# Performance work log

Hardware: AMD Instinct MI355X
Metric: run time of the kernel (lower is better)

## Reference

```python
import jax, jax.numpy as jnp
import numpy as np
from jax import lax

NB_ITERS = 10
HS = 3        # nb_kerhalfsize
HS_LIF = 3    # nb_kerhalfsize_LIF
DN = ('NCDHW', 'OIDHW', 'NCDHW')


def std_kernel(sigma, halfsize):
    # sigma: (C,1,1,1) -> normalized Gaussian kernel (C,1,k,k,k)
    r = jnp.arange(-halfsize, halfsize + 1, dtype=jnp.float32)
    x, y, z = jnp.meshgrid(r, r, r, indexing='ij')  # (k,k,k)
    d2 = x ** 2 + y ** 2 + z ** 2
    sig2 = sigma.reshape(-1, 1, 1, 1) ** 2          # (C,1,1,1)
    ker = jnp.exp(-d2[None] / (2.0 * sig2))         # (C,k,k,k)
    ker = ker / (ker.sum(axis=(1, 2, 3), keepdims=True) + 1e-15)
    return ker[:, None]                              # (C,1,k,k,k)


def dconv(x, ker, halfsize):
    # depthwise (grouped, groups=C) 3D conv with 'same' zero padding
    C = x.shape[1]
    pad = [(halfsize, halfsize)] * 3
    return lax.conv_general_dilated(x, ker, window_strides=(1, 1, 1),
                                    padding=pad, feature_group_count=C,
                                    dimension_numbers=DN)


def setup_inputs() -> dict:
    key = jax.random.key(0)
    k1, k2 = jax.random.split(key)
    C = 4
    shape = (1, C, 96, 96, 96)
    o = jax.random.normal(k1, shape, dtype=jnp.float32)
    I = jax.random.uniform(k2, (1, 1, 96, 96, 96), dtype=jnp.float32)
    sigma2 = jnp.ones((C, 1, 1, 1), dtype=jnp.float32)
    sigma3 = jnp.ones((C, 1, 1, 1), dtype=jnp.float32)
    eta = jnp.ones((1,), dtype=jnp.float32)
    lam = jnp.ones((1,), dtype=jnp.float32) * 5.0
    mu = jnp.ones((1,), dtype=jnp.float32) * 5.0
    return {'o': o, 'I': I, 'sigma2': sigma2, 'sigma3': sigma3,
            'eta': eta, 'lam': lam, 'mu': mu}


def reference(o, I, sigma2, sigma3, eta, lam, mu):
    u = jax.nn.softmax(o / eta, axis=1)
    ker = std_kernel(sigma2, HS)
    ker_lif = std_kernel(sigma3, HS_LIF)
    # conv of the all-ones tensor is loop-invariant (boundary normalization)
    conv_ones = dconv(jnp.ones_like(u), ker_lif, HS_LIF)
    I2 = I ** 2
    for _ in range(NB_ITERS):
        uI = u * I
        C1 = dconv(uI, ker_lif, HS_LIF)
        C2 = dconv(u, ker_lif, HS_LIF)
        Cn = (C1 + 1e-6) / (C2 + 1e-6)
        Lif = (dconv(Cn ** 2, ker_lif, HS_LIF)
               - 2.0 * I * dconv(Cn, ker_lif, HS_LIF)
               + I2 * conv_ones)
        q = dconv(1.0 - 2.0 * u, ker, HS)
        u = jax.nn.softmax((o - mu * Lif - lam * q) / eta, axis=1)
    return u
```

## Files before the change

### kernel.cpp

```cpp
#include <hip/hip_runtime.h>
#include <math.h>

#define PLANE  9216
#define PLANE4 2304
#define VOL    884736
#define VOL4   221184
#define NC     4
#define K      7
#define HSR    3
#define SEGZ   8
#define NSEGZ  12
#define SEGZ4  16
#define NSEGZ4 6

#define YT     16
#define YTH    22
#define TPBYX  192
#define LINW   100
#define MIDW   108
#define NF4    528

__device__ __forceinline__ float4 f4zero() { return make_float4(0.f, 0.f, 0.f, 0.f); }
__device__ __forceinline__ float4 f4fma(float t, float4 a, float4 s) {
    s.x = fmaf(t, a.x, s.x); s.y = fmaf(t, a.y, s.y);
    s.z = fmaf(t, a.z, s.z); s.w = fmaf(t, a.w, s.w);
    return s;
}
__device__ __forceinline__ float4 f4fmasq(float t, float4 a, float4 s) {
    s.x = fmaf(t, a.x * a.x, s.x); s.y = fmaf(t, a.y * a.y, s.y);
    s.z = fmaf(t, a.z * a.z, s.z); s.w = fmaf(t, a.w * a.w, s.w);
    return s;
}
__device__ __forceinline__ float4 f4mul(float4 a, float4 b) {
    return make_float4(a.x * b.x, a.y * b.y, a.z * b.z, a.w * b.w);
}

__global__ void tables_kernel(const float* __restrict__ sigma2,
                              const float* __restrict__ sigma3,
                              float* __restrict__ taps2, float* __restrict__ taps3,
                              float* __restrict__ B2, float* __restrict__ B3)
{
    int t = threadIdx.x;
    if (t < 2 * NC) {
        int c = t % NC;
        const float* sig = (t < NC) ? sigma2 : sigma3;
        float* taps = (t < NC) ? taps2 : taps3;
        float sv = sig[c];
        float s2 = sv * sv;
        float w[K];
        float sum = 0.f;
        for (int j = 0; j < K; j++) {
            float d = (float)(j - HSR);
            w[j] = expf(-d * d / (2.f * s2));
            sum += w[j];
        }
        float inv = 1.f / sum;
        for (int j = 0; j < K; j++) taps[c * K + j] = w[j] * inv;
    }
    __syncthreads();
    for (int i = t; i < NC * 96; i += blockDim.x) {
        int c = i / 96, p = i % 96;
        float s2v = 0.f, s3v = 0.f;
        for (int j = 0; j < K; j++) {
            int q = p + j - HSR;
            if (q >= 0 && q < 96) { s2v += taps2[c * K + j]; s3v += taps3[c * K + j]; }
        }
        B2[i] = s2v;
        B3[i] = s3v;
    }
}

__global__ __launch_bounds__(256) void softmax_kernel(const float* __restrict__ a,
                                                      const float* __restrict__ eta,
                                                      float* __restrict__ u)
{
    int i = blockIdx.x * 256 + threadIdx.x;
    const float4* A = (const float4*)a;
    float4* U = (float4*)u;
    float inv_eta = 1.f / eta[0];
    float4 a0 = A[i], a1 = A[i + VOL4], a2 = A[i + 2 * VOL4], a3 = A[i + 3 * VOL4];
#define SM_COMP(f)                                                              \
    {                                                                           \
        float b0 = a0.f * inv_eta, b1 = a1.f * inv_eta;                         \
        float b2 = a2.f * inv_eta, b3 = a3.f * inv_eta;                         \
        float m = fmaxf(fmaxf(b0, b1), fmaxf(b2, b3));                          \
        float e0 = __expf(b0 - m), e1 = __expf(b1 - m);                         \
        float e2 = __expf(b2 - m), e3 = __expf(b3 - m);                         \
        float inv = 1.f / (e0 + e1 + e2 + e3);                                  \
        a0.f = e0 * inv; a1.f = e1 * inv; a2.f = e2 * inv; a3.f = e3 * inv;     \
    }
    SM_COMP(x) SM_COMP(y) SM_COMP(z) SM_COMP(w)
    U[i] = a0; U[i + VOL4] = a1; U[i + 2 * VOL4] = a2; U[i + 3 * VOL4] = a3;
}

__global__ __launch_bounds__(256) void pass1_z(const float* __restrict__ u,
                                               const float* __restrict__ I,
                                               const float* __restrict__ taps2,
                                               const float* __restrict__ taps3,
                                               float* __restrict__ a0, float* __restrict__ a1,
                                               float* __restrict__ a2)
{
    int p4 = blockIdx.x * 256 + threadIdx.x;
    int s  = blockIdx.y;
    int c  = blockIdx.z;
    int z0 = s * SEGZ;
    const float4* ub = (const float4*)(u + (size_t)c * VOL) + p4;
    const float4* Ib = (const float4*)I + p4;
    float t3[K], t2[K];
#pragma unroll
    for (int j = 0; j < K; j++) { t3[j] = taps3[c * K + j]; t2[j] = taps2[c * K + j]; }
    float4 wu[K], wui[K];
#pragma unroll
    for (int j = 0; j < K - 1; j++) {
        int z = z0 + j - HSR;
        float4 uv = f4zero(), iv = f4zero();
        if (z >= 0 && z < 96) { uv = ub[z * PLANE4]; iv = Ib[z * PLANE4]; }
        wu[j] = uv; wui[j] = f4mul(uv, iv);
    }
    float4* o0 = (float4*)(a0 + (size_t)c * VOL) + p4;
    float4* o1 = (float4*)(a1 + (size_t)c * VOL) + p4;
    float4* o2 = (float4*)(a2 + (size_t)c * VOL) + p4;
    for (int k = 0; k < SEGZ; k++) {
        int z = z0 + k, zl = z + HSR;
        float4 uv = f4zero(), iv = f4zero();
        if (zl < 96) { uv = ub[zl * PLANE4]; iv = Ib[zl * PLANE4]; }
        wu[K - 1] = uv; wui[K - 1] = f4mul(uv, iv);
        float4 s0 = f4zero(), s1 = f4zero(), s2 = f4zero();
#pragma unroll
        for (int j = 0; j < K; j++) {
            s0 = f4fma(t3[j], wui[j], s0);
            s1 = f4fma(t3[j], wu[j], s1);
            s2 = f4fma(t2[j], wu[j], s2);
        }
        o0[z * PLANE4] = s0;
        o1[z * PLANE4] = s1;
        o2[z * PLANE4] = s2;
#pragma unroll
        for (int j = 0; j < K - 1; j++) { wu[j] = wu[j + 1]; wui[j] = wui[j + 1]; }
    }
}

__global__ __launch_bounds__(TPBYX) void pass2_yx(const float* __restrict__ a0,
                                                  const float* __restrict__ a1,
                                                  const float* __restrict__ taps3,
                                                  float* __restrict__ Cn)
{
    __shared__ float lin[2][YTH * LINW];
    __shared__ float mid[2][YT * MIDW];
    int yt = blockIdx.x, z = blockIdx.y, c = blockIdx.z;
    int y0 = yt * YT, tid = threadIdx.x;
    size_t base = (size_t)c * VOL + (size_t)z * PLANE;
    {
        const float4* g0 = (const float4*)(a0 + base);
        const float4* g1 = (const float4*)(a1 + base);
#pragma unroll
        for (int i4 = tid; i4 < NF4; i4 += TPBYX) {
            int r = i4 / 24, k = i4 - r * 24;
            int gy = y0 - HSR + r;
            bool ok = (gy >= 0 && gy < 96);
            int gi = gy * 24 + k;
            float4 v0 = ok ? g0[gi] : f4zero();
            float4 v1 = ok ? g1[gi] : f4zero();
            int li = r * LINW + k * 4;
            *(float4*)&lin[0][li] = v0;
            *(float4*)&lin[1][li] = v1;
        }
    }
    if (tid < 128) {
        int r = tid >> 3, p = tid & 7;
        int idx = r * MIDW + (p < 4 ? p : 96 + p);
        mid[0][idx] = 0.f; mid[1][idx] = 0.f;
    }
    float t3[K];
#pragma unroll
    for (int j = 0; j < K; j++) t3[j] = taps3[c * K + j];
    __syncthreads();
    int r  = tid / 12;
    int xb = (tid - r * 12) * 8;
#pragma unroll
    for (int f = 0; f < 2; f++) {
        float4 mA = f4zero(), mB = f4zero();
#pragma unroll
        for (int j = 0; j < K; j++) {
            const float4* lp = (const float4*)&lin[f][(r + j) * LINW + xb];
            mA = f4fma(t3[j], lp[0], mA);
            mB = f4fma(t3[j], lp[1], mB);
        }
        float4* mp = (float4*)&mid[f][r * MIDW + 4 + xb];
        mp[0] = mA; mp[1] = mB;
    }
    __syncthreads();
    float outA[8], outB[8];
    {
        float wf[16];
#pragma unroll
        for (int f = 0; f < 2; f++) {
            const float4* wp = (const float4*)&mid[f][r * MIDW + xb];
            *(float4*)&wf[0]  = wp[0];
            *(float4*)&wf[4]  = wp[1];
            *(float4*)&wf[8]  = wp[2];
            *(float4*)&wf[12] = wp[3];
            float* dst = (f == 0) ? outA : outB;
#pragma unroll
            for (int k = 0; k < 8; k++) {
                float s = 0.f;
#pragma unroll
                for (int j = 0; j < K; j++) s = fmaf(t3[j], wf[k + j + 1], s);
                dst[k] = s;
            }
        }
    }
    int y = y0 + r;
    float co[8];
#pragma unroll
    for (int k = 0; k < 8; k++)
        co[k] = (outA[k] + 1e-6f) / (outB[k] + 1e-6f);
    float* cp = Cn + base + y * 96 + xb;
    *(float4*)cp       = *(float4*)&co[0];
    *(float4*)(cp + 4) = *(float4*)&co[4];
}

__global__ __launch_bounds__(128) void pass4_z(const float* __restrict__ Cn,
                                               const float* __restrict__ taps3,
                                               float* __restrict__ b0, float* __restrict__ b1)
{
    int p4 = blockIdx.x * 128 + threadIdx.x;
    int s  = blockIdx.y;
    int c  = blockIdx.z;
    int z0 = s * SEGZ4;
    const float4* ib = (const float4*)(Cn + (size_t)c * VOL) + p4;
    float t3[K];
#pragma unroll
    for (int j = 0; j < K; j++) t3[j] = taps3[c * K + j];
    float4 w[K];
#pragma unroll
    for (int j = 0; j < K - 1; j++) {
        int z = z0 + j - HSR;
        float4 v = f4zero();
        if (z >= 0 && z < 96) v = ib[z * PLANE4];
        w[j] = v;
    }
    float4* o0 = (float4*)(b0 + (size_t)c * VOL) + p4;
    float4* o1 = (float4*)(b1 + (size_t)c * VOL) + p4;
    for (int k = 0; k < SEGZ4; k++) {
        int z = z0 + k, zl = z + HSR;
        float4 v = f4zero();
        if (zl < 96) v = ib[zl * PLANE4];
        w[K - 1] = v;
        float4 s0 = f4zero(), s1 = f4zero();
#pragma unroll
        for (int j = 0; j < K; j++) {
            s0 = f4fma(t3[j], w[j], s0);
            s1 = f4fmasq(t3[j], w[j], s1);
        }
        o0[z * PLANE4] = s0;
        o1[z * PLANE4] = s1;
#pragma unroll
        for (int j = 0; j < K - 1; j++) w[j] = w[j + 1];
    }
}

__global__ __launch_bounds__(TPBYX) void pass5_yx(const float* __restrict__ cz0,
                                                  const float* __restrict__ cz1,
                                                  const float* __restrict__ a2,
                                                  const float* __restrict__ o,
                                                  const float* __restrict__ I,
                                                  const float* __restrict__ taps2,
                                                  const float* __restrict__ taps3,
                                                  const float* __restrict__ B2,
                                                  const float* __restrict__ B3,
                                                  const float* __restrict__ eta,
                                                  const float* __restrict__ lam,
                                                  const float* __restrict__ mu,
                                                  float* __restrict__ argb)
{
    __shared__ float lin[3][YTH * LINW];
    __shared__ float mid[3][YT * MIDW];
    int yt = blockIdx.x, z = blockIdx.y, c = blockIdx.z;
    int y0 = yt * YT, tid = threadIdx.x;
    size_t base = (size_t)c * VOL + (size_t)z * PLANE;
    {
        const float4* g0 = (const float4*)(cz0 + base);
        const float4* g1 = (const float4*)(cz1 + base);
        const float4* g2 = (const float4*)(a2 + base);
#pragma unroll
        for (int i4 = tid; i4 < NF4; i4 += TPBYX) {
            int r = i4 / 24, k = i4 - r * 24;
            int gy = y0 - HSR + r;
            bool ok = (gy >= 0 && gy < 96);
            int gi = gy * 24 + k;
            float4 v0 = ok ? g0[gi] : f4zero();
            float4 v1 = ok ? g1[gi] : f4zero();
            float4 v2 = ok ? g2[gi] : f4zero();
            int li = r * LINW + k * 4;
            *(float4*)&lin[0][li] = v0;
            *(float4*)&lin[1][li] = v1;
            *(float4*)&lin[2][li] = v2;
        }
    }
    if (tid < 128) {
        int r = tid >> 3, p = tid & 7;
        int idx = r * MIDW + (p < 4 ? p : 96 + p);
        mid[0][idx] = 0.f; mid[1][idx] = 0.f; mid[2][idx] = 0.f;
    }
    float t3[K], t2[K];
#pragma unroll
    for (int j = 0; j < K; j++) { t3[j] = taps3[c * K + j]; t2[j] = taps2[c * K + j]; }
    __syncthreads();
    int r  = tid / 12;
    int xb = (tid - r * 12) * 8;
#pragma unroll
    for (int f = 0; f < 3; f++) {
        const float* tp = (f < 2) ? t3 : t2;
        float4 mA = f4zero(), mB = f4zero();
#pragma unroll
        for (int j = 0; j < K; j++) {
            const float4* lp = (const float4*)&lin[f][(r + j) * LINW + xb];
            mA = f4fma(tp[j], lp[0], mA);
            mB = f4fma(tp[j], lp[1], mB);
        }
        float4* mp = (float4*)&mid[f][r * MIDW + 4 + xb];
        mp[0] = mA; mp[1] = mB;
    }
    __syncthreads();
    float d0[8], d1[8], s2[8];
    {
        float wf[16];
#pragma unroll
        for (int f = 0; f < 3; f++) {
            const float* tp = (f < 2) ? t3 : t2;
            const float4* wp = (const float4*)&mid[f][r * MIDW + xb];
            *(float4*)&wf[0]  = wp[0];
            *(float4*)&wf[4]  = wp[1];
            *(float4*)&wf[8]  = wp[2];
            *(float4*)&wf[12] = wp[3];
            float* dst = (f == 0) ? d0 : (f == 1) ? d1 : s2;
#pragma unroll
            for (int k = 0; k < 8; k++) {
                float s = 0.f;
#pragma unroll
                for (int j = 0; j < K; j++) s = fmaf(tp[j], wf[k + j + 1], s);
                dst[k] = s;
            }
        }
    }
    int y = y0 + r;
    int v = z * PLANE + y * 96 + xb;
    float inv_eta = 1.f / eta[0];
    float lamv = lam[0], muv = mu[0];
    float Bz3 = B3[c * 96 + z], By3 = B3[c * 96 + y];
    float Bz2 = B2[c * 96 + z], By2 = B2[c * 96 + y];
    float Bx3[8], Bx2[8], Ivv[8], ov[8];
    {
        const float4* bx3 = (const float4*)&B3[c * 96 + xb];
        *(float4*)&Bx3[0] = bx3[0]; *(float4*)&Bx3[4] = bx3[1];
        const float4* bx2 = (const float4*)&B2[c * 96 + xb];
        *(float4*)&Bx2[0] = bx2[0]; *(float4*)&Bx2[4] = bx2[1];
        const float4* ip = (const float4*)&I[v];
        *(float4*)&Ivv[0] = ip[0]; *(float4*)&Ivv[4] = ip[1];
        const float4* op = (const float4*)&o[(size_t)c * VOL + v];
        *(float4*)&ov[0] = op[0]; *(float4*)&ov[4] = op[1];
    }
    float res[8];
#pragma unroll
    for (int k = 0; k < 8; k++) {
        float Iv = Ivv[k];
        float cones = Bz3 * By3 * Bx3[k];
        float Lif = d1[k] - 2.f * Iv * d0[k] + Iv * Iv * cones;
        float qv  = fmaf(Bz2 * By2, Bx2[k], -2.f * s2[k]);
        res[k] = ov[k] - muv * Lif - lamv * qv;
    }
    float* ap = argb + base + y * 96 + xb;
    *(float4*)ap       = *(float4*)&res[0];
    *(float4*)(ap + 4) = *(float4*)&res[4];
}

extern "C" void kernel_launch(void* const* d_in, const int* in_sizes, int n_in,
                              void* d_out, int out_size, void* d_ws, size_t ws_size,
                              hipStream_t stream)
{
    const float* o      = (const float*)d_in[0];
    const float* I      = (const float*)d_in[1];
    const float* sigma2 = (const float*)d_in[2];
    const float* sigma3 = (const float*)d_in[3];
    const float* eta    = (const float*)d_in[4];
    const float* lam    = (const float*)d_in[5];
    const float* mu     = (const float*)d_in[6];
    float* u = (float*)d_out;

    float* wsf = (float*)d_ws;
    float* taps2 = wsf;
    float* taps3 = wsf + 32;
    float* B2    = wsf + 64;
    float* B3    = wsf + 64 + NC * 96;
    float* buf   = wsf + 1024;
    const size_t VCs = (size_t)NC * VOL;
    float* a0 = buf;
    float* a1 = buf + VCs;
    float* a2 = buf + 2 * VCs;
    float* Cn = buf + 3 * VCs;
    float* c0 = buf + 4 * VCs;
    float* c1 = buf + 5 * VCs;

    const dim3 grid1(PLANE4 / 256, NSEGZ, NC);
    const dim3 gridYX(96 / YT, 96, NC);
    const dim3 grid4(PLANE4 / 128, NSEGZ4, NC);
    const int gridV4 = VOL4 / 256;

    tables_kernel<<<1, 512, 0, stream>>>(sigma2, sigma3, taps2, taps3, B2, B3);
    softmax_kernel<<<gridV4, 256, 0, stream>>>(o, eta, u);
    for (int it = 0; it < 10; it++) {
        pass1_z<<<grid1, 256, 0, stream>>>(u, I, taps2, taps3, a0, a1, a2);
        pass2_yx<<<gridYX, TPBYX, 0, stream>>>(a0, a1, taps3, Cn);
        pass4_z<<<grid4, 128, 0, stream>>>(Cn, taps3, c0, c1);
        pass5_yx<<<gridYX, TPBYX, 0, stream>>>(c0, c1, a2, o, I, taps2, taps3,
                                               B2, B3, eta, lam, mu, a0);
        softmax_kernel<<<gridV4, 256, 0, stream>>>(a0, eta, u);
    }
}
```

Baseline: 714.9 us.

## Fuse y and x conv passes in registers, drop mid shared buffer

The separable y and x convolutions in the yx kernels now run in registers. Each thread accumulates a 16-wide y-convolved window straight from the padded line buffer, then applies the x taps, so the intermediate shared array and one barrier are gone. The line buffer gains zero halos on both sides to support this. The z-pass also moves to 256-thread blocks with 8-slice segments, which doubles the halo reloads per output. The per-thread y pass does 16 columns instead of 8, so it adds redundant FMAs and register pressure.

```diff
diff --git a/kernel.cpp b/kernel.cpp
--- a/kernel.cpp
+++ b/kernel.cpp
@@ -10,14 +10,11 @@
 #define HSR    3
 #define SEGZ   8
 #define NSEGZ  12
-#define SEGZ4  16
-#define NSEGZ4 6
 
 #define YT     16
 #define YTH    22
 #define TPBYX  192
-#define LINW   100
-#define MIDW   108
+#define LINW   108
 #define NF4    528
 
 __device__ __forceinline__ float4 f4zero() { return make_float4(0.f, 0.f, 0.f, 0.f); }
@@ -33,6 +30,36 @@
 }
 __device__ __forceinline__ float4 f4mul(float4 a, float4 b) {
     return make_float4(a.x * b.x, a.y * b.y, a.z * b.z, a.w * b.w);
+}
+
+__device__ __forceinline__ void conv_win(const float* __restrict__ linf,
+                                         const float* __restrict__ tp,
+                                         int r, int xb, float out[8])
+{
+    float acc[16];
+#pragma unroll
+    for (int i = 0; i < 16; i++) acc[i] = 0.f;
+#pragma unroll
+    for (int j = 0; j < K; j++) {
+        const float4* lp = (const float4*)&linf[(r + j) * LINW + xb];
+        float4 w0 = lp[0], w1 = lp[1], w2 = lp[2], w3 = lp[3];
+        float t = tp[j];
+        acc[0]  = fmaf(t, w0.x, acc[0]);  acc[1]  = fmaf(t, w0.y, acc[1]);
+        acc[2]  = fmaf(t, w0.z, acc[2]);  acc[3]  = fmaf(t, w0.w, acc[3]);
+        acc[4]  = fmaf(t, w1.x, acc[4]);  acc[5]  = fmaf(t, w1.y, acc[5]);
+        acc[6]  = fmaf(t, w1.z, acc[6]);  acc[7]  = fmaf(t, w1.w, acc[7]);
+        acc[8]  = fmaf(t, w2.x, acc[8]);  acc[9]  = fmaf(t, w2.y, acc[9]);
+        acc[10] = fmaf(t, w2.z, acc[10]); acc[11] = fmaf(t, w2.w, acc[11]);
+        acc[12] = fmaf(t, w3.x, acc[12]); acc[13] = fmaf(t, w3.y, acc[13]);
+        acc[14] = fmaf(t, w3.z, acc[14]); acc[15] = fmaf(t, w3.w, acc[15]);
+    }
+#pragma unroll
+    for (int k = 0; k < 8; k++) {
+        float s = 0.f;
+#pragma unroll
+        for (int j = 0; j < K; j++) s = fmaf(tp[j], acc[k + j + 1], s);
+        out[k] = s;
+    }
 }
 
 __global__ void tables_kernel(const float* __restrict__ sigma2,
@@ -146,7 +173,6 @@
                                                   float* __restrict__ Cn)
 {
     __shared__ float lin[2][YTH * LINW];
-    __shared__ float mid[2][YT * MIDW];
     int yt = blockIdx.x, z = blockIdx.y, c = blockIdx.z;
     int y0 = yt * YT, tid = threadIdx.x;
     size_t base = (size_t)c * VOL + (size_t)z * PLANE;
@@ -161,15 +187,15 @@
             int gi = gy * 24 + k;
             float4 v0 = ok ? g0[gi] : f4zero();
             float4 v1 = ok ? g1[gi] : f4zero();
-            int li = r * LINW + k * 4;
+            int li = r * LINW + 4 + k * 4;
             *(float4*)&lin[0][li] = v0;
             *(float4*)&lin[1][li] = v1;
         }
     }
-    if (tid < 128) {
+    if (tid < YTH * 8) {
         int r = tid >> 3, p = tid & 7;
-        int idx = r * MIDW + (p < 4 ? p : 96 + p);
-        mid[0][idx] = 0.f; mid[1][idx] = 0.f;
+        int idx = r * LINW + (p < 4 ? p : 96 + p);
+        lin[0][idx] = 0.f; lin[1][idx] = 0.f;
     }
     float t3[K];
 #pragma unroll
@@ -177,39 +203,9 @@
     __syncthreads();
     int r  = tid / 12;
     int xb = (tid - r * 12) * 8;
-#pragma unroll
-    for (int f = 0; f < 2; f++) {
-        float4 mA = f4zero(), mB = f4zero();
-#pragma unroll
-        for (int j = 0; j < K; j++) {
-            const float4* lp = (const float4*)&lin[f][(r + j) * LINW + xb];
-            mA = f4fma(t3[j], lp[0], mA);
-            mB = f4fma(t3[j], lp[1], mB);
-        }
-        float4* mp = (float4*)&mid[f][r * MIDW + 4 + xb];
-        mp[0] = mA; mp[1] = mB;
-    }
-    __syncthreads();
     float outA[8], outB[8];
-    {
-        float wf[16];
-#pragma unroll
-        for (int f = 0; f < 2; f++) {
-            const float4* wp = (const float4*)&mid[f][r * MIDW + xb];
-            *(float4*)&wf[0]  = wp[0];
-            *(float4*)&wf[4]  = wp[1];
-            *(float4*)&wf[8]  = wp[2];
-            *(float4*)&wf[12] = wp[3];
-            float* dst = (f == 0) ? outA : outB;
-#pragma unroll
-            for (int k = 0; k < 8; k++) {
-                float s = 0.f;
-#pragma unroll
-                for (int j = 0; j < K; j++) s = fmaf(t3[j], wf[k + j + 1], s);
-                dst[k] = s;
-            }
-        }
-    }
+    conv_win(lin[0], t3, r, xb, outA);
+    conv_win(lin[1], t3, r, xb, outB);
     int y = y0 + r;
     float co[8];
 #pragma unroll
@@ -220,14 +216,14 @@
     *(float4*)(cp + 4) = *(float4*)&co[4];
 }
 
-__global__ __launch_bounds__(128) void pass4_z(const float* __restrict__ Cn,
+__global__ __launch_bounds__(256) void pass4_z(const float* __restrict__ Cn,
                                                const float* __restrict__ taps3,
                                                float* __restrict__ b0, float* __restrict__ b1)
 {
-    int p4 = blockIdx.x * 128 + threadIdx.x;
+    int p4 = blockIdx.x * 256 + threadIdx.x;
     int s  = blockIdx.y;
     int c  = blockIdx.z;
-    int z0 = s * SEGZ4;
+    int z0 = s * SEGZ;
     const float4* ib = (const float4*)(Cn + (size_t)c * VOL) + p4;
     float t3[K];
 #pragma unroll
@@ -242,7 +238,7 @@
     }
     float4* o0 = (float4*)(b0 + (size_t)c * VOL) + p4;
     float4* o1 = (float4*)(b1 + (size_t)c * VOL) + p4;
-    for (int k = 0; k < SEGZ4; k++) {
+    for (int k = 0; k < SEGZ; k++) {
         int z = z0 + k, zl = z + HSR;
         float4 v = f4zero();
         if (zl < 96) v = ib[zl * PLANE4];
@@ -269,13 +265,11 @@
                                                   const float* __restrict__ taps3,
                                                   const float* __restrict__ B2,
                                                   const float* __restrict__ B3,
-                                                  const float* __restrict__ eta,
                                                   const float* __restrict__ lam,
                                                   const float* __restrict__ mu,
                                                   float* __restrict__ argb)
 {
     __shared__ float lin[3][YTH * LINW];
-    __shared__ float mid[3][YT * MIDW];
     int yt = blockIdx.x, z = blockIdx.y, c = blockIdx.z;
     int y0 = yt * YT, tid = threadIdx.x;
     size_t base = (size_t)c * VOL + (size_t)z * PLANE;
@@ -292,16 +286,16 @@
             float4 v0 = ok ? g0[gi] : f4zero();
             float4 v1 = ok ? g1[gi] : f4zero();
             float4 v2 = ok ? g2[gi] : f4zero();
-            int li = r * LINW + k * 4;
+            int li = r * LINW + 4 + k * 4;
             *(float4*)&lin[0][li] = v0;
             *(float4*)&lin[1][li] = v1;
             *(float4*)&lin[2][li] = v2;
         }
     }
-    if (tid < 128) {
+    if (tid < YTH * 8) {
         int r = tid >> 3, p = tid & 7;
-        int idx = r * MIDW + (p < 4 ? p : 96 + p);
-        mid[0][idx] = 0.f; mid[1][idx] = 0.f; mid[2][idx] = 0.f;
+        int idx = r * LINW + (p < 4 ? p : 96 + p);
+        lin[0][idx] = 0.f; lin[1][idx] = 0.f; lin[2][idx] = 0.f;
     }
     float t3[K], t2[K];
 #pragma unroll
@@ -309,44 +303,12 @@
     __syncthreads();
     int r  = tid / 12;
     int xb = (tid - r * 12) * 8;
-#pragma unroll
-    for (int f = 0; f < 3; f++) {
-        const float* tp = (f < 2) ? t3 : t2;
-        float4 mA = f4zero(), mB = f4zero();
-#pragma unroll
-        for (int j = 0; j < K; j++) {
-            const float4* lp = (const float4*)&lin[f][(r + j) * LINW + xb];
-            mA = f4fma(tp[j], lp[0], mA);
-            mB = f4fma(tp[j], lp[1], mB);
-        }
-        float4* mp = (float4*)&mid[f][r * MIDW + 4 + xb];
-        mp[0] = mA; mp[1] = mB;
-    }
-    __syncthreads();
     float d0[8], d1[8], s2[8];
-    {
-        float wf[16];
-#pragma unroll
-        for (int f = 0; f < 3; f++) {
-            const float* tp = (f < 2) ? t3 : t2;
-            const float4* wp = (const float4*)&mid[f][r * MIDW + xb];
-            *(float4*)&wf[0]  = wp[0];
-            *(float4*)&wf[4]  = wp[1];
-            *(float4*)&wf[8]  = wp[2];
-            *(float4*)&wf[12] = wp[3];
-            float* dst = (f == 0) ? d0 : (f == 1) ? d1 : s2;
-#pragma unroll
-            for (int k = 0; k < 8; k++) {
-                float s = 0.f;
-#pragma unroll
-                for (int j = 0; j < K; j++) s = fmaf(tp[j], wf[k + j + 1], s);
-                dst[k] = s;
-            }
-        }
-    }
+    conv_win(lin[0], t3, r, xb, d0);
+    conv_win(lin[1], t3, r, xb, d1);
+    conv_win(lin[2], t2, r, xb, s2);
     int y = y0 + r;
     int v = z * PLANE + y * 96 + xb;
-    float inv_eta = 1.f / eta[0];
     float lamv = lam[0], muv = mu[0];
     float Bz3 = B3[c * 96 + z], By3 = B3[c * 96 + y];
     float Bz2 = B2[c * 96 + z], By2 = B2[c * 96 + y];
@@ -402,19 +364,18 @@
     float* c0 = buf + 4 * VCs;
     float* c1 = buf + 5 * VCs;
 
-    const dim3 grid1(PLANE4 / 256, NSEGZ, NC);
+    const dim3 gridZ(PLANE4 / 256, NSEGZ, NC);
     const dim3 gridYX(96 / YT, 96, NC);
-    const dim3 grid4(PLANE4 / 128, NSEGZ4, NC);
     const int gridV4 = VOL4 / 256;
 
     tables_kernel<<<1, 512, 0, stream>>>(sigma2, sigma3, taps2, taps3, B2, B3);
     softmax_kernel<<<gridV4, 256, 0, stream>>>(o, eta, u);
     for (int it = 0; it < 10; it++) {
-        pass1_z<<<grid1, 256, 0, stream>>>(u, I, taps2, taps3, a0, a1, a2);
+        pass1_z<<<gridZ, 256, 0, stream>>>(u, I, taps2, taps3, a0, a1, a2);
         pass2_yx<<<gridYX, TPBYX, 0, stream>>>(a0, a1, taps3, Cn);
-        pass4_z<<<grid4, 128, 0, stream>>>(Cn, taps3, c0, c1);
+        pass4_z<<<gridZ, 256, 0, stream>>>(Cn, taps3, c0, c1);
         pass5_yx<<<gridYX, TPBYX, 0, stream>>>(c0, c1, a2, o, I, taps2, taps3,
-                                               B2, B3, eta, lam, mu, a0);
+                                               B2, B3, lam, mu, a0);
         softmax_kernel<<<gridV4, 256, 0, stream>>>(a0, eta, u);
     }
 }
```

Result: slower. 1.025 ms (+43.4%).
